# Kernel tuning notes

Measured on AMD Instinct MI355X. Metric: run time of the kernel, lower is better.

The kernel has to match this reference:

```python
import jax, jax.numpy as jnp
import numpy as np

WORD_VOCAB, WORD_DIM = 50257, 512
CHAR_VOCAB, CHAR_DIM = 262, 128
OUT_DIM = 1024
B, SW, SC = 32, 256, 16
EMB_DIM = WORD_DIM + CHAR_DIM


def setup_inputs() -> dict:
    key = jax.random.key(0)
    ks = jax.random.split(key, 12)
    word_inputs = jax.random.randint(ks[0], (B, SW), 0, WORD_VOCAB)
    char_ids = jax.random.randint(ks[1], (B, SW, SC), 0, CHAR_VOCAB)
    char_lengths = jax.random.randint(ks[2], (B, SW), 1, SC + 1)  # at least 1 char
    word_table = jax.random.normal(ks[3], (WORD_VOCAB, WORD_DIM), jnp.float32) * 0.02
    char_table = jax.random.normal(ks[4], (CHAR_VOCAB, CHAR_DIM), jnp.float32) * 0.02
    # RecursiveCell: gate = Linear(2d -> 3d), project = Linear(2d -> d)
    Wg = jax.random.normal(ks[5], (3 * CHAR_DIM, 2 * CHAR_DIM), jnp.float32) * (1.0 / np.sqrt(2 * CHAR_DIM))
    bg = jnp.zeros((3 * CHAR_DIM,), jnp.float32)
    Wp = jax.random.normal(ks[6], (CHAR_DIM, 2 * CHAR_DIM), jnp.float32) * (1.0 / np.sqrt(2 * CHAR_DIM))
    bp = jnp.zeros((CHAR_DIM,), jnp.float32)
    # final projection Linear(emb_dim -> output_dim)
    W_out = jax.random.normal(ks[7], (OUT_DIM, EMB_DIM), jnp.float32) * (1.0 / np.sqrt(EMB_DIM))
    b_out = jnp.zeros((OUT_DIM,), jnp.float32)
    return {"word_inputs": word_inputs, "char_ids": char_ids, "char_lengths": char_lengths,
            "word_table": word_table, "char_table": char_table,
            "Wg": Wg, "bg": bg, "Wp": Wp, "bp": bp, "W_out": W_out, "b_out": b_out}


def reference(word_inputs, char_ids, char_lengths, word_table, char_table, Wg, bg, Wp, bp, W_out, b_out):
    b, sw = word_inputs.shape
    sc = char_ids.shape[-1]
    d = char_table.shape[-1]
    n = b * sw

    word_emb = word_table[word_inputs]                      # [B, SW, WORD_DIM]

    ids = char_ids.reshape(n, sc)
    lens = char_lengths.reshape(n, 1)
    layer0 = char_table[ids]                                # [N, SC, d]
    pos = jnp.arange(sc)

    def step(layer, length):
        # vectorized RecursiveCell over all adjacent pairs i in [0, SC-2]
        left = layer[:, :-1, :]                             # [N, SC-1, d]
        right = layer[:, 1:, :]                             # [N, SC-1, d]
        flat = jnp.concatenate([left, right], axis=-1)      # [N, SC-1, 2d]
        z = flat @ Wp.T + bp                                # [N, SC-1, d]
        g = jax.nn.softmax((flat @ Wg.T + bg).reshape(n, sc - 1, 3, d), axis=2)
        ret = g[:, :, 0] * left + g[:, :, 1] * right + g[:, :, 2] * z
        new_layer = jnp.pad(ret, ((0, 0), (0, 1), (0, 0)))  # positions >= SC-1 stay zero
        # masked_scatter_: update position i iff i < len - length
        mask = (pos[None, :] < (lens - length))[..., None]  # [N, SC, 1]
        return jnp.where(mask, new_layer, layer), None

    layer, _ = jax.lax.scan(step, layer0, jnp.arange(1, sc))
    char_repr = layer[:, 0, :].reshape(b, sw, d)            # [B, SW, d]

    token_embedding = jnp.concatenate([word_emb, char_repr], axis=-1)
    return token_embedding @ W_out.T + b_out                # [B, SW, OUT_DIM]
```

## Files before the change

### kernel.cpp

```cpp
#include <hip/hip_runtime.h>
#include <hip/hip_bf16.h>

#define NTOK 8192
#define SCC  16
#define CD   128
#define WD   512
#define OD   1024
#define ED   640
#define TW   4

typedef __attribute__((ext_vector_type(8))) short short8;
typedef __attribute__((ext_vector_type(4))) float f32x4;

__device__ __forceinline__ unsigned short f2bf(float f) {
    union { float f; unsigned u; } v; v.f = f;
    unsigned r = v.u + 0x7FFF + ((v.u >> 16) & 1);
    return (unsigned short)(r >> 16);
}

__global__ void sort_zero(int* s) { if (threadIdx.x < 48) s[threadIdx.x] = 0; }

__global__ void sort_hist(const int* __restrict__ lengths, int* __restrict__ s) {
    const int i = blockIdx.x * 256 + threadIdx.x;
    if (i < NTOK) atomicAdd(&s[lengths[i] - 1], 1);
}

__global__ void sort_prefix(int* s) {
    if (threadIdx.x == 0) {
        int acc = 0;
        for (int b = 15; b >= 0; --b) { s[16 + b] = acc; acc += s[b]; }
    }
}

__global__ __launch_bounds__(256) void sort_scatter_det(
    const int* __restrict__ lengths, int* __restrict__ s)
{
    __shared__ int wsum[4];
    __shared__ int running;
    const int b   = blockIdx.x;
    const int tid = threadIdx.x;
    if (tid == 0) running = s[16 + b];
    __syncthreads();
    for (int c0 = 0; c0 < NTOK; c0 += 256) {
        const int i = c0 + tid;
        const bool f = (lengths[i] - 1 == b);
        const unsigned long long m = __ballot(f);
        const int wv = tid >> 6;
        if ((tid & 63) == 0) wsum[wv] = __popcll(m);
        __syncthreads();
        int excl = 0;
#pragma unroll
        for (int k = 0; k < 4; ++k) if (k < wv) excl += wsum[k];
        const int lanerank = __popcll(m & ((1ull << (tid & 63)) - 1ull));
        if (f) s[48 + running + excl + lanerank] = i;
        const int tot = wsum[0] + wsum[1] + wsum[2] + wsum[3];
        __syncthreads();
        if (tid == 0) running += tot;
        __syncthreads();
    }
}

__global__ __launch_bounds__(256) void pack_weights(
    const float* __restrict__ Wg, const float* __restrict__ Wp,
    uint4* __restrict__ packed)
{
    const int gid  = blockIdx.x * 256 + threadIdx.x;
    const int lane = gid & 63;
    const int kf   = (gid >> 6) & 7;
    const int c    = (gid >> 9) & 3;
    const int w    = (gid >> 11) & 7;
    const int n    = c * 128 + w * 16 + (lane & 15);
    const int k0   = kf * 32 + (lane >> 4) * 8;
    const float* src = (n < 384) ? (Wg + n * 256 + k0) : (Wp + (n - 384) * 256 + k0);
    uint4 o;
    o.x = f2bf(src[0]) | ((unsigned)f2bf(src[1]) << 16);
    o.y = f2bf(src[2]) | ((unsigned)f2bf(src[3]) << 16);
    o.z = f2bf(src[4]) | ((unsigned)f2bf(src[5]) << 16);
    o.w = f2bf(src[6]) | ((unsigned)f2bf(src[7]) << 16);
    packed[gid] = o;
}

__global__ __launch_bounds__(256) void pack_wout(
    const float* __restrict__ W_out, uint4* __restrict__ packed)
{
    const int gid  = blockIdx.x * 256 + threadIdx.x;
    const int lane = gid & 63;
    const int kf   = (gid >> 6) % 20;
    const int nb   = (gid >> 6) / 20;
    const int n    = nb * 16 + (lane & 15);
    const int k0   = kf * 32 + (lane >> 4) * 8;
    const float* src = W_out + (size_t)n * ED + k0;
    uint4 o;
    o.x = f2bf(src[0]) | ((unsigned)f2bf(src[1]) << 16);
    o.y = f2bf(src[2]) | ((unsigned)f2bf(src[3]) << 16);
    o.z = f2bf(src[4]) | ((unsigned)f2bf(src[5]) << 16);
    o.w = f2bf(src[6]) | ((unsigned)f2bf(src[7]) << 16);
    packed[gid] = o;
}

#define LOAD_B(DST, KF)                                                     \
    {                                                                       \
        const uint4* wp_ = Wpacked + (w * 32 + (KF)) * 64 + lane;           \
        union { uint4 u; short8 s; } cv0, cv1, cv2, cv3;                    \
        cv0.u = wp_[0];    DST[0] = cv0.s;                                  \
        cv1.u = wp_[512];  DST[1] = cv1.s;                                  \
        cv2.u = wp_[1024]; DST[2] = cv2.s;                                  \
        cv3.u = wp_[1536]; DST[3] = cv3.s;                                  \
    }

#define LOAD_B_LDS(DST, KFI)                                                \
    {                                                                       \
        const uint4* sp_ = SW + ((w * 3 + (KFI)) * 4) * 64 + lane;          \
        union { uint4 u; short8 s; } d0, d1, d2, d3;                        \
        d0.u = sp_[0];   DST[0] = d0.s;                                     \
        d1.u = sp_[64];  DST[1] = d1.s;                                     \
        d2.u = sp_[128]; DST[2] = d2.s;                                     \
        d3.u = sp_[192]; DST[3] = d3.s;                                     \
    }

#define MFMA_PHASE(BV, KF)                                                  \
    {                                                                       \
        _Pragma("unroll")                                                   \
        for (int m_ = 0; m_ < 4; ++m_) {                                    \
            if (m_ < mfrags) {                                              \
                const int r_ = m_ * 16 + col + (((KF) >= 4) ? 4 : 0);       \
                int ba_ = (r_ << 8) + (((KF) & 3) << 6) + (q << 4);         \
                ba_ ^= (r_ & 15) << 4;                                      \
                const short8 a_ = *reinterpret_cast<const short8*>(         \
                    reinterpret_cast<const char*>(X) + ba_);                \
                acc[m_][0] = __builtin_amdgcn_mfma_f32_16x16x32_bf16(a_, BV[0], acc[m_][0], 0, 0, 0); \
                acc[m_][1] = __builtin_amdgcn_mfma_f32_16x16x32_bf16(a_, BV[1], acc[m_][1], 0, 0, 0); \
                acc[m_][2] = __builtin_amdgcn_mfma_f32_16x16x32_bf16(a_, BV[2], acc[m_][2], 0, 0, 0); \
                acc[m_][3] = __builtin_amdgcn_mfma_f32_16x16x32_bf16(a_, BV[3], acc[m_][3], 0, 0, 0); \
            }                                                               \
        }                                                                   \
    }

__global__ __launch_bounds__(512, 2) void scan_mfma(
    const int*   __restrict__ char_ids,
    const int*   __restrict__ char_lengths,
    const float* __restrict__ char_table,
    const float* __restrict__ bg, const float* __restrict__ bp,
    const uint4* __restrict__ Wpacked,
    const int*   __restrict__ order,
    unsigned short* __restrict__ char_repr)
{
    __shared__ __align__(16) unsigned short X[68 * 128];
    __shared__ __align__(16) uint4 SW[8 * 3 * 4 * 64];
    __shared__ int toksh[TW];
    __shared__ int Lsh[TW];

    const int tid  = threadIdx.x;
    const int lane = tid & 63;
    const int w    = tid >> 6;
    const int col  = lane & 15;
    const int q    = lane >> 4;

    if (tid < TW) {
        const int tok = order[blockIdx.x * TW + tid];
        toksh[tid] = tok;
        Lsh[tid]   = char_lengths[tok];
    }

    const int dj = w * 16 + col;
    const float b02 = bg[dj] - bg[256 + dj];
    const float b12 = bg[128 + dj] - bg[256 + dj];
    const float bz  = bp[dj];

    short8 bpin0[4], bpin1[4];
    LOAD_B(bpin0, 0);
    LOAD_B(bpin1, 1);

#pragma unroll
    for (int kfi = 0; kfi < 3; ++kfi)
#pragma unroll
        for (int c = 0; c < 4; ++c)
            SW[((w * 3 + kfi) * 4 + c) * 64 + lane] =
                Wpacked[(w * 32 + c * 8 + (2 + kfi)) * 64 + lane];

    __syncthreads();

    int L[TW];
#pragma unroll
    for (int i = 0; i < TW; ++i) L[i] = Lsh[i];
    const int maxL = max(max(L[0], L[1]), max(L[2], L[3]));

    float stv[4][4];
#pragma unroll
    for (int m = 0; m < 4; ++m) {
        const int p = m * 4 + q;
#pragma unroll
        for (int i = 0; i < 4; ++i) {
            const int id = char_ids[toksh[i] * SCC + p];
            stv[m][i] = char_table[id * CD + dj];
        }
    }

#pragma unroll
    for (int m = 0; m < 4; ++m)
#pragma unroll
        for (int i = 0; i < 4; ++i) {
            const int rl = m * 16 + q * 4 + i;
            int bl = (rl << 8) + (dj << 1);
            bl ^= (rl & 15) << 4;
            *reinterpret_cast<unsigned short*>(reinterpret_cast<char*>(X) + bl) =
                f2bf(stv[m][i]);
        }
    for (int i2 = tid; i2 < 4 * 64; i2 += 512) {
        const int r = 64 + (i2 >> 6), ku = i2 & 63;
        int ba = (r << 8) + (ku << 2);
        ba ^= (r & 15) << 4;
        *reinterpret_cast<unsigned*>(reinterpret_cast<char*>(X) + ba) = 0u;
    }
    __syncthreads();

    for (int len = 1; len < maxL; ++len) {
        const int Amax   = maxL - len;
        const int mfrags = (4 * Amax + 15) >> 4;

        f32x4 acc[4][4];
#pragma unroll
        for (int m = 0; m < 4; ++m)
#pragma unroll
            for (int c = 0; c < 4; ++c) acc[m][c] = (f32x4){0.f, 0.f, 0.f, 0.f};

        short8 bA[4], bB[4], bL[4];
        LOAD_B(bA, 5);
        LOAD_B(bB, 6);
        MFMA_PHASE(bpin0, 0);
        LOAD_B_LDS(bL, 0);
        MFMA_PHASE(bpin1, 1);
        MFMA_PHASE(bL, 2);
        LOAD_B_LDS(bL, 1);
        MFMA_PHASE(bL, 3);
        LOAD_B_LDS(bL, 2);
        MFMA_PHASE(bL, 4);
        MFMA_PHASE(bA, 5);
        LOAD_B(bA, 7);
        MFMA_PHASE(bB, 6);
        MFMA_PHASE(bA, 7);

        float shifted[5][4];
#pragma unroll
        for (int m = 0; m < 4; ++m)
#pragma unroll
            for (int i = 0; i < 4; ++i)
                shifted[m][i] = __shfl(stv[m][i], (lane + 16) & 63);
#pragma unroll
        for (int i = 0; i < 4; ++i) shifted[4][i] = 0.f;

#pragma unroll
        for (int m = 0; m < 4; ++m) {
            if (m < mfrags) {
                const int p = m * 4 + q;
#pragma unroll
                for (int i = 0; i < 4; ++i) {
                    const float a0  = acc[m][0][i];
                    const float a1  = acc[m][1][i];
                    const float a2v = acc[m][2][i];
                    const float z   = acc[m][3][i] + bz;
                    const float E0  = __expf(a0 - a2v + b02);
                    const float E1  = __expf(a1 - a2v + b12);
                    const float left  = stv[m][i];
                    const float right = (q < 3) ? shifted[m][i] : shifted[m + 1][i];
                    const float inv = __builtin_amdgcn_rcpf(E0 + E1 + 1.0f);
                    const float nv  = (E0 * left + E1 * right + z) * inv;
                    stv[m][i] = (p < L[i] - len) ? nv : stv[m][i];
                }
            }
        }
        __syncthreads();

#pragma unroll
        for (int m = 0; m < 4; ++m) {
            if (m < mfrags) {
#pragma unroll
                for (int i = 0; i < 4; ++i) {
                    const int rl = m * 16 + q * 4 + i;
                    int bl = (rl << 8) + (dj << 1);
                    bl ^= (rl & 15) << 4;
                    *reinterpret_cast<unsigned short*>(
                        reinterpret_cast<char*>(X) + bl) = f2bf(stv[m][i]);
                }
            }
        }
        __syncthreads();
    }

    if (q == 0) {
#pragma unroll
        for (int i = 0; i < 4; ++i)
            char_repr[toksh[i] * CD + dj] = f2bf(stv[0][i]);
    }
}

#define TPB2 32

__global__ __launch_bounds__(512) void out_mfma(
    const int*   __restrict__ word_inputs,
    const float* __restrict__ word_table,
    const unsigned short* __restrict__ char_repr,
    const uint4* __restrict__ pwout,
    const float* __restrict__ b_out,
    float*       __restrict__ out)
{
    __shared__ __align__(16) unsigned short E[TPB2 * ED];

    const int tg   = blockIdx.x * TPB2;
    const int tid  = threadIdx.x;
    const int lane = tid & 63;
    const int w    = tid >> 6;
    const int col  = lane & 15;
    const int q    = lane >> 4;

    for (int i = tid; i < TPB2 * 256; i += 512) {
        const int rt = i >> 8, kp = i & 255;
        const float2 v = *reinterpret_cast<const float2*>(
            word_table + (size_t)word_inputs[tg + rt] * WD + 2 * kp);
        const unsigned u = f2bf(v.x) | ((unsigned)f2bf(v.y) << 16);
        int baddr = rt * 1280 + kp * 4;
        baddr ^= (rt & 7) << 4;
        *reinterpret_cast<unsigned*>(reinterpret_cast<char*>(E) + baddr) = u;
    }
    for (int i = tid; i < TPB2 * 64; i += 512) {
        const int rt = i >> 6, kp = i & 63;
        const unsigned u = *reinterpret_cast<const unsigned*>(
            char_repr + (tg + rt) * CD + 2 * kp);
        int baddr = rt * 1280 + 1024 + kp * 4;
        baddr ^= (rt & 7) << 4;
        *reinterpret_cast<unsigned*>(reinterpret_cast<char*>(E) + baddr) = u;
    }
    __syncthreads();

    f32x4 acc[2][8];
#pragma unroll
    for (int mm = 0; mm < 2; ++mm)
#pragma unroll
        for (int nf = 0; nf < 8; ++nf) acc[mm][nf] = (f32x4){0.f, 0.f, 0.f, 0.f};

#pragma unroll 4
    for (int kf = 0; kf < 20; ++kf) {
        short8 a[2];
#pragma unroll
        for (int mm = 0; mm < 2; ++mm) {
            const int row = mm * 16 + col;
            int ba = row * 1280 + kf * 64 + q * 16;
            ba ^= (row & 7) << 4;
            a[mm] = *reinterpret_cast<const short8*>(
                reinterpret_cast<const char*>(E) + ba);
        }
#pragma unroll
        for (int nf = 0; nf < 8; ++nf) {
            const int nb = w * 8 + nf;
            union { uint4 u; short8 s; } cv;
            cv.u = pwout[(nb * 20 + kf) * 64 + lane];
            acc[0][nf] = __builtin_amdgcn_mfma_f32_16x16x32_bf16(a[0], cv.s, acc[0][nf], 0, 0, 0);
            acc[1][nf] = __builtin_amdgcn_mfma_f32_16x16x32_bf16(a[1], cv.s, acc[1][nf], 0, 0, 0);
        }
    }

#pragma unroll
    for (int nf = 0; nf < 8; ++nf) {
        const int j = (w * 8 + nf) * 16 + col;
        const float bias = b_out[j];
#pragma unroll
        for (int mm = 0; mm < 2; ++mm)
#pragma unroll
            for (int i = 0; i < 4; ++i) {
                out[(size_t)(tg + mm * 16 + q * 4 + i) * OD + j] = acc[mm][nf][i] + bias;
            }
    }
}


extern "C" void kernel_launch(void* const* d_in, const int* in_sizes, int n_in,
                              void* d_out, int out_size, void* d_ws, size_t ws_size,
                              hipStream_t stream)
{
    const int*   word_inputs  = (const int*)  d_in[0];
    const int*   char_ids     = (const int*)  d_in[1];
    const int*   char_lengths = (const int*)  d_in[2];
    const float* word_table   = (const float*)d_in[3];
    const float* char_table   = (const float*)d_in[4];
    const float* Wg           = (const float*)d_in[5];
    const float* bg           = (const float*)d_in[6];
    const float* Wp           = (const float*)d_in[7];
    const float* bp           = (const float*)d_in[8];
    const float* W_out        = (const float*)d_in[9];
    const float* b_out        = (const float*)d_in[10];

    float* out = (float*)d_out;
    char* ws = (char*)d_ws;
    unsigned short* char_repr = (unsigned short*)ws;
    uint4* Wpacked = (uint4*)(ws + 2 * 1024 * 1024);
    int*   sortbuf = (int*)(ws + 2 * 1024 * 1024 + 256 * 1024);
    const int* order = sortbuf + 48;
    uint4* pwout = (uint4*)(ws + 2 * 1024 * 1024 + 256 * 1024 + 64 * 1024);

    pack_weights<<<64, 256, 0, stream>>>(Wg, Wp, Wpacked);
    pack_wout<<<320, 256, 0, stream>>>(W_out, pwout);
    sort_zero<<<1, 64, 0, stream>>>(sortbuf);
    sort_hist<<<NTOK / 256, 256, 0, stream>>>(char_lengths, sortbuf);
    sort_prefix<<<1, 64, 0, stream>>>(sortbuf);
    sort_scatter_det<<<16, 256, 0, stream>>>(char_lengths, sortbuf);

    scan_mfma<<<NTOK / TW, 512, 0, stream>>>(char_ids, char_lengths, char_table,
                                             bg, bp, Wpacked, order, char_repr);
    out_mfma<<<NTOK / TPB2, 512, 0, stream>>>(word_inputs, word_table, char_repr,
                                              pwout, b_out, out);
}
```

Measured before the change: 267.8 us.

## Process eight words per scan block with two-half MFMA passes

The recursive char-scan kernel now handles eight tokens per block instead of four. The state layout is remapped so each 16-row fragment holds two positions times eight tokens, and the step loop runs a first and optional second MFMA half with its own shuffle and update. The aim is to amortise the weight fragments held in registers and LDS, and the per-step barriers, over twice as many tokens, halving the block count. The cost is more registers, larger LDS use for X, and a per-block maxL taken over more tokens, so short words wait on the longest one.

```diff
diff --git a/kernel.cpp b/kernel.cpp
--- a/kernel.cpp
+++ b/kernel.cpp
@@ -7,7 +7,7 @@
 #define WD   512
 #define OD   1024
 #define ED   640
-#define TW   4
+#define TW   8
 
 typedef __attribute__((ext_vector_type(8))) short short8;
 typedef __attribute__((ext_vector_type(4))) float f32x4;
@@ -118,12 +118,12 @@
         d3.u = sp_[192]; DST[3] = d3.s;                                     \
     }
 
-#define MFMA_PHASE(BV, KF)                                                  \
+#define MFMA_PHASE(BV, KF, MB, MF)                                          \
     {                                                                       \
         _Pragma("unroll")                                                   \
         for (int m_ = 0; m_ < 4; ++m_) {                                    \
-            if (m_ < mfrags) {                                              \
-                const int r_ = m_ * 16 + col + (((KF) >= 4) ? 4 : 0);       \
+            if (m_ < (MF)) {                                                \
+                const int r_ = ((MB) + m_) * 16 + col + (((KF) >= 4) ? 8 : 0); \
                 int ba_ = (r_ << 8) + (((KF) & 3) << 6) + (q << 4);         \
                 ba_ ^= (r_ & 15) << 4;                                      \
                 const short8 a_ = *reinterpret_cast<const short8*>(         \
@@ -136,6 +136,25 @@
         }                                                                   \
     }
 
+#define MFMA_HALF(MB, MF)                                                   \
+    {                                                                       \
+        short8 bA[4], bB[4], bL[4];                                         \
+        LOAD_B(bA, 5);                                                      \
+        LOAD_B(bB, 6);                                                      \
+        MFMA_PHASE(bpin0, 0, MB, MF);                                       \
+        LOAD_B_LDS(bL, 0);                                                  \
+        MFMA_PHASE(bpin1, 1, MB, MF);                                       \
+        MFMA_PHASE(bL, 2, MB, MF);                                          \
+        LOAD_B_LDS(bL, 1);                                                  \
+        MFMA_PHASE(bL, 3, MB, MF);                                          \
+        LOAD_B_LDS(bL, 2);                                                  \
+        MFMA_PHASE(bL, 4, MB, MF);                                          \
+        MFMA_PHASE(bA, 5, MB, MF);                                          \
+        LOAD_B(bA, 7);                                                      \
+        MFMA_PHASE(bB, 6, MB, MF);                                          \
+        MFMA_PHASE(bA, 7, MB, MF);                                          \
+    }
+
 __global__ __launch_bounds__(512, 2) void scan_mfma(
     const int*   __restrict__ char_ids,
     const int*   __restrict__ char_lengths,
@@ -145,7 +164,7 @@
     const int*   __restrict__ order,
     unsigned short* __restrict__ char_repr)
 {
-    __shared__ __align__(16) unsigned short X[68 * 128];
+    __shared__ __align__(16) unsigned short X[136 * 128];
     __shared__ __align__(16) uint4 SW[8 * 3 * 4 * 64];
     __shared__ int toksh[TW];
     __shared__ int Lsh[TW];
@@ -155,6 +174,8 @@
     const int w    = tid >> 6;
     const int col  = lane & 15;
     const int q    = lane >> 4;
+    const int qh   = q >> 1;
+    const int ql   = q & 1;
 
     if (tid < TW) {
         const int tok = order[blockIdx.x * TW + tid];
@@ -180,24 +201,26 @@
 
     __syncthreads();
 
-    int L[TW];
-#pragma unroll
-    for (int i = 0; i < TW; ++i) L[i] = Lsh[i];
-    const int maxL = max(max(L[0], L[1]), max(L[2], L[3]));
-
-    float stv[4][4];
-#pragma unroll
-    for (int m = 0; m < 4; ++m) {
-        const int p = m * 4 + q;
+    int Lme[4], tokme[4];
+#pragma unroll
+    for (int i = 0; i < 4; ++i) { Lme[i] = Lsh[ql * 4 + i]; tokme[i] = toksh[ql * 4 + i]; }
+    int maxL = Lsh[0];
+#pragma unroll
+    for (int j = 1; j < TW; ++j) maxL = max(maxL, Lsh[j]);
+
+    float stv[8][4];
+#pragma unroll
+    for (int m = 0; m < 8; ++m) {
+        const int p = 2 * m + qh;
 #pragma unroll
         for (int i = 0; i < 4; ++i) {
-            const int id = char_ids[toksh[i] * SCC + p];
+            const int id = char_ids[tokme[i] * SCC + p];
             stv[m][i] = char_table[id * CD + dj];
         }
     }
 
 #pragma unroll
-    for (int m = 0; m < 4; ++m)
+    for (int m = 0; m < 8; ++m)
 #pragma unroll
         for (int i = 0; i < 4; ++i) {
             const int rl = m * 16 + q * 4 + i;
@@ -206,8 +229,8 @@
             *reinterpret_cast<unsigned short*>(reinterpret_cast<char*>(X) + bl) =
                 f2bf(stv[m][i]);
         }
-    for (int i2 = tid; i2 < 4 * 64; i2 += 512) {
-        const int r = 64 + (i2 >> 6), ku = i2 & 63;
+    {
+        const int r = 128 + (tid >> 6), ku = tid & 63;
         int ba = (r << 8) + (ku << 2);
         ba ^= (r & 15) << 4;
         *reinterpret_cast<unsigned*>(reinterpret_cast<char*>(X) + ba) = 0u;
@@ -216,81 +239,125 @@
 
     for (int len = 1; len < maxL; ++len) {
         const int Amax   = maxL - len;
-        const int mfrags = (4 * Amax + 15) >> 4;
-
-        f32x4 acc[4][4];
-#pragma unroll
-        for (int m = 0; m < 4; ++m)
-#pragma unroll
-            for (int c = 0; c < 4; ++c) acc[m][c] = (f32x4){0.f, 0.f, 0.f, 0.f};
-
-        short8 bA[4], bB[4], bL[4];
-        LOAD_B(bA, 5);
-        LOAD_B(bB, 6);
-        MFMA_PHASE(bpin0, 0);
-        LOAD_B_LDS(bL, 0);
-        MFMA_PHASE(bpin1, 1);
-        MFMA_PHASE(bL, 2);
-        LOAD_B_LDS(bL, 1);
-        MFMA_PHASE(bL, 3);
-        LOAD_B_LDS(bL, 2);
-        MFMA_PHASE(bL, 4);
-        MFMA_PHASE(bA, 5);
-        LOAD_B(bA, 7);
-        MFMA_PHASE(bB, 6);
-        MFMA_PHASE(bA, 7);
-
-        float shifted[5][4];
-#pragma unroll
-        for (int m = 0; m < 4; ++m)
-#pragma unroll
-            for (int i = 0; i < 4; ++i)
-                shifted[m][i] = __shfl(stv[m][i], (lane + 16) & 63);
-#pragma unroll
-        for (int i = 0; i < 4; ++i) shifted[4][i] = 0.f;
-
-#pragma unroll
-        for (int m = 0; m < 4; ++m) {
-            if (m < mfrags) {
-                const int p = m * 4 + q;
-#pragma unroll
-                for (int i = 0; i < 4; ++i) {
-                    const float a0  = acc[m][0][i];
-                    const float a1  = acc[m][1][i];
-                    const float a2v = acc[m][2][i];
-                    const float z   = acc[m][3][i] + bz;
-                    const float E0  = __expf(a0 - a2v + b02);
-                    const float E1  = __expf(a1 - a2v + b12);
-                    const float left  = stv[m][i];
-                    const float right = (q < 3) ? shifted[m][i] : shifted[m + 1][i];
-                    const float inv = __builtin_amdgcn_rcpf(E0 + E1 + 1.0f);
-                    const float nv  = (E0 * left + E1 * right + z) * inv;
-                    stv[m][i] = (p < L[i] - len) ? nv : stv[m][i];
+        const int mf_tot = (Amax + 1) >> 1;
+        const int mfrags = (mf_tot < 4) ? mf_tot : 4;
+        const bool dual  = (mf_tot > 4);
+
+        {
+            f32x4 acc[4][4];
+#pragma unroll
+            for (int m = 0; m < 4; ++m)
+#pragma unroll
+                for (int c = 0; c < 4; ++c) acc[m][c] = (f32x4){0.f, 0.f, 0.f, 0.f};
+
+            MFMA_HALF(0, mfrags);
+            __syncthreads();
+
+            float sh0[5][4];
+#pragma unroll
+            for (int m = 0; m < 5; ++m)
+#pragma unroll
+                for (int i = 0; i < 4; ++i)
+                    sh0[m][i] = __shfl(stv[m][i], (lane + 32) & 63);
+
+#pragma unroll
+            for (int m = 0; m < 4; ++m) {
+                if (m < mfrags) {
+                    const int p = 2 * m + qh;
+#pragma unroll
+                    for (int i = 0; i < 4; ++i) {
+                        const float a0  = acc[m][0][i];
+                        const float a1  = acc[m][1][i];
+                        const float a2v = acc[m][2][i];
+                        const float z   = acc[m][3][i] + bz;
+                        const float E0  = __expf(a0 - a2v + b02);
+                        const float E1  = __expf(a1 - a2v + b12);
+                        const float left  = stv[m][i];
+                        const float right = (qh == 0) ? sh0[m][i] : sh0[m + 1][i];
+                        const float inv = __builtin_amdgcn_rcpf(E0 + E1 + 1.0f);
+                        const float nv  = (E0 * left + E1 * right + z) * inv;
+                        stv[m][i] = (p < Lme[i] - len) ? nv : stv[m][i];
+                    }
                 }
             }
-        }
-        __syncthreads();
-
-#pragma unroll
-        for (int m = 0; m < 4; ++m) {
-            if (m < mfrags) {
-#pragma unroll
-                for (int i = 0; i < 4; ++i) {
-                    const int rl = m * 16 + q * 4 + i;
-                    int bl = (rl << 8) + (dj << 1);
-                    bl ^= (rl & 15) << 4;
-                    *reinterpret_cast<unsigned short*>(
-                        reinterpret_cast<char*>(X) + bl) = f2bf(stv[m][i]);
+#pragma unroll
+            for (int m = 0; m < 4; ++m) {
+                if (m < mfrags) {
+#pragma unroll
+                    for (int i = 0; i < 4; ++i) {
+                        const int rl = m * 16 + q * 4 + i;
+                        int bl = (rl << 8) + (dj << 1);
+                        bl ^= (rl & 15) << 4;
+                        *reinterpret_cast<unsigned short*>(
+                            reinterpret_cast<char*>(X) + bl) = f2bf(stv[m][i]);
+                    }
                 }
             }
         }
-        __syncthreads();
-    }
-
-    if (q == 0) {
+
+        if (dual) {
+            const int mfrags2 = mf_tot - 4;
+            f32x4 acc[4][4];
+#pragma unroll
+            for (int m = 0; m < 4; ++m)
+#pragma unroll
+                for (int c = 0; c < 4; ++c) acc[m][c] = (f32x4){0.f, 0.f, 0.f, 0.f};
+
+            MFMA_HALF(4, mfrags2);
+            __syncthreads();
+
+            float sh1[5][4];
+#pragma unroll
+            for (int m = 0; m < 4; ++m)
+#pragma unroll
+                for (int i = 0; i < 4; ++i)
+                    sh1[m][i] = __shfl(stv[4 + m][i], (lane + 32) & 63);
+#pragma unroll
+            for (int i = 0; i < 4; ++i) sh1[4][i] = 0.f;
+
+#pragma unroll
+            for (int m = 0; m < 4; ++m) {
+                if (m < mfrags2) {
+                    const int p = 2 * (4 + m) + qh;
+#pragma unroll
+                    for (int i = 0; i < 4; ++i) {
+                        const float a0  = acc[m][0][i];
+                        const float a1  = acc[m][1][i];
+                        const float a2v = acc[m][2][i];
+                        const float z   = acc[m][3][i] + bz;
+                        const float E0  = __expf(a0 - a2v + b02);
+                        const float E1  = __expf(a1 - a2v + b12);
+                        const float left  = stv[4 + m][i];
+                        const float right = (qh == 0) ? sh1[m][i] : sh1[m + 1][i];
+                        const float inv = __builtin_amdgcn_rcpf(E0 + E1 + 1.0f);
+                        const float nv  = (E0 * left + E1 * right + z) * inv;
+                        stv[4 + m][i] = (p < Lme[i] - len) ? nv : stv[4 + m][i];
+                    }
+                }
+            }
+#pragma unroll
+            for (int m = 0; m < 4; ++m) {
+                if (m < mfrags2) {
+#pragma unroll
+                    for (int i = 0; i < 4; ++i) {
+                        const int rl = (4 + m) * 16 + q * 4 + i;
+                        int bl = (rl << 8) + (dj << 1);
+                        bl ^= (rl & 15) << 4;
+                        *reinterpret_cast<unsigned short*>(
+                            reinterpret_cast<char*>(X) + bl) = f2bf(stv[4 + m][i]);
+                    }
+                }
+            }
+            __syncthreads();
+        } else {
+            __syncthreads();
+        }
+    }
+
+    if (q < 2) {
 #pragma unroll
         for (int i = 0; i < 4; ++i)
-            char_repr[toksh[i] * CD + dj] = f2bf(stv[0][i]);
+            char_repr[tokme[i] * CD + dj] = f2bf(stv[0][i]);
     }
 }
 
```

New measurement: 618.0 us. 131% more time.
